# Performance work log

Hardware: AMD Instinct MI355X
Metric: run time of the kernel (lower is better)

Reference implementation:

```python
import jax, jax.numpy as jnp
import numpy as np

N_NODES = 50000
N_EDGES = 600000
D_IN = 256    # hidden_lstm
D_GNN = 128   # hidden_gnn
D_OUT = 1     # out_channels


def setup_inputs() -> dict:
    key = jax.random.key(0)
    ks = jax.random.split(key, 8)
    x = jax.random.normal(ks[0], (N_NODES, D_IN), dtype=jnp.float32)
    edge_index = jax.random.randint(ks[1], (2, N_EDGES), 0, N_NODES, dtype=jnp.int32)
    # SAGEConv params: lin_l applied to aggregated neighbors (with bias), lin_r to root
    s_in = 1.0 / np.sqrt(D_IN)
    W_l = jax.random.uniform(ks[2], (D_IN, D_GNN), jnp.float32, -s_in, s_in)
    b_l = jax.random.uniform(ks[3], (D_GNN,), jnp.float32, -s_in, s_in)
    W_r = jax.random.uniform(ks[4], (D_IN, D_GNN), jnp.float32, -s_in, s_in)
    # fc head
    s_g = 1.0 / np.sqrt(D_GNN)
    W_fc = jax.random.uniform(ks[5], (D_GNN, D_OUT), jnp.float32, -s_g, s_g)
    b_fc = jax.random.uniform(ks[6], (D_OUT,), jnp.float32, -s_g, s_g)
    return {"x": x, "edge_index": edge_index, "W_l": W_l, "b_l": b_l,
            "W_r": W_r, "W_fc": W_fc, "b_fc": b_fc}


def reference(x, edge_index, W_l, b_l, W_r, W_fc, b_fc):
    # SAGEConv, aggr='mean': out = lin_l(mean_{j in N(i)} x_j) + lin_r(x_i)
    src = edge_index[0]  # message source
    dst = edge_index[1]  # message target
    n = x.shape[0]
    agg = jax.ops.segment_sum(x[src], dst, num_segments=n)            # [N, D_IN]
    cnt = jax.ops.segment_sum(jnp.ones((src.shape[0], 1), x.dtype), dst,
                              num_segments=n)                         # [N, 1]
    mean = agg / jnp.maximum(cnt, 1.0)
    h = mean @ W_l + b_l + x @ W_r                                    # [N, D_GNN]
    pred = jax.nn.sigmoid(h @ W_fc + b_fc).squeeze()                  # [N]
    return h, pred
```

## Files before the change

### kernel.cpp

```cpp
#include <hip/hip_runtime.h>
#include <hip/hip_bf16.h>
#include <math.h>

#define N_NODES 50000
#define N_EDGES 600000
#define D_IN 256
#define D_GNN 128
#define CAP 32
#define MAX_OVER 8192
#define LDS_STRIDE 264

typedef short s16x8 __attribute__((ext_vector_type(8)));
typedef float f32x4 __attribute__((ext_vector_type(4)));

__device__ __forceinline__ unsigned short f2bf(float f) {
  unsigned int u = __float_as_uint(f);
  u += 0x7FFFu + ((u >> 16) & 1u);
  return (unsigned short)(u >> 16);
}

__device__ __forceinline__ ushort4 cvt4(float4 a) {
  union { ushort4 u4; __hip_bfloat162 h[2]; } u;
  u.h[0] = __float22bfloat162_rn(make_float2(a.x, a.y));
  u.h[1] = __float22bfloat162_rn(make_float2(a.z, a.w));
  return u.u4;
}

__global__ __launch_bounds__(256) void pack0(
    const float* __restrict__ Wl, const float* __restrict__ Wr,
    ushort* __restrict__ Wcp, int* __restrict__ cursor,
    int* __restrict__ ovcnt) {
  int i = blockIdx.x * 256 + threadIdx.x;
  if (i < N_NODES) cursor[i] = 0;
  if (i == 0) ovcnt[0] = 0;
  if (i < 8192) {
    int q = i & 3, col = (i >> 2) & 255, ks = i >> 10;
    const float* W = (col < 128) ? Wl : Wr;
    int c = col & 127;
    int k0 = ks * 32 + q * 8;
    s16x8 v;
#pragma unroll
    for (int j = 0; j < 8; j++) v[j] = (short)f2bf(W[(k0 + j) * D_GNN + c]);
    *((s16x8*)(Wcp + (size_t)i * 8)) = v;
  }
}

__global__ __launch_bounds__(256) void fill_pad(
    const int* __restrict__ ei, int* __restrict__ cursor,
    int* __restrict__ colp, int* __restrict__ ovcnt, int2* __restrict__ over) {
  int e = blockIdx.x * 256 + threadIdx.x;
  if (e >= N_EDGES) return;
  int src = ei[e];
  int dst = ei[N_EDGES + e];
  int pos = atomicAdd(&cursor[dst], 1);
  if (pos < CAP) {
    colp[dst * CAP + pos] = src;
  } else {
    int o = atomicAdd(ovcnt, 1);
    if (o < MAX_OVER) over[o] = make_int2(dst, src);
  }
}

__global__ __launch_bounds__(512) void mfma_gemm(
    const float* __restrict__ x, const ushort* __restrict__ Wcp,
    const float* __restrict__ b_l, ushort* __restrict__ yb,
    ushort* __restrict__ yrb) {
  __shared__ ushort xs[64 * LDS_STRIDE];
  const int t = threadIdx.x;
  const int n0 = blockIdx.x * 64;

#pragma unroll
  for (int j = 0; j < 8; j++) {
    int idx = t + j * 512;
    int row = idx >> 6, col4 = idx & 63;
    int gn = n0 + row;
    if (gn >= N_NODES) gn = N_NODES - 1;
    float4 v = ((const float4*)x)[(size_t)gn * 64 + col4];
    *((ushort4*)(xs + row * LDS_STRIDE + col4 * 4)) = cvt4(v);
  }
  __syncthreads();

  const int l = t & 63;
  const int w = t >> 6;
  const int wrow = w & 1;
  const int wcol = w >> 1;
  const int lq = l >> 4, l16 = l & 15;

  f32x4 acc[2][4];
#pragma unroll
  for (int a = 0; a < 2; a++)
#pragma unroll
    for (int b = 0; b < 4; b++) acc[a][b] = (f32x4){0.f, 0.f, 0.f, 0.f};

  const ushort* abase[2];
#pragma unroll
  for (int nt = 0; nt < 2; nt++)
    abase[nt] = xs + (wrow * 32 + nt * 16 + l16) * LDS_STRIDE + lq * 8;
  const ushort* bptr[4];
#pragma unroll
  for (int ct = 0; ct < 4; ct++) {
    int col = wcol * 64 + ct * 16 + l16;
    bptr[ct] = Wcp + ((size_t)col * 4 + lq) * 8;
  }

  s16x8 B[4], Bn[4];
#pragma unroll
  for (int ct = 0; ct < 4; ct++) B[ct] = *((const s16x8*)(bptr[ct]));

#pragma unroll
  for (int ks = 0; ks < 8; ks++) {
    s16x8 A[2];
#pragma unroll
    for (int nt = 0; nt < 2; nt++)
      A[nt] = *((const s16x8*)(abase[nt] + ks * 32));
    if (ks < 7) {
#pragma unroll
      for (int ct = 0; ct < 4; ct++)
        Bn[ct] = *((const s16x8*)(bptr[ct] + (size_t)(ks + 1) * 256 * 32));
    }
#pragma unroll
    for (int nt = 0; nt < 2; nt++)
#pragma unroll
      for (int ct = 0; ct < 4; ct++)
        acc[nt][ct] = __builtin_amdgcn_mfma_f32_16x16x32_bf16(
            A[nt], B[ct], acc[nt][ct], 0, 0, 0);
#pragma unroll
    for (int ct = 0; ct < 4; ct++) B[ct] = Bn[ct];
  }

#pragma unroll
  for (int nt = 0; nt < 2; nt++) {
#pragma unroll
    for (int ct = 0; ct < 4; ct++) {
      int gcol = wcol * 64 + ct * 16 + l16;
#pragma unroll
      for (int r = 0; r < 4; r++) {
        int node = n0 + wrow * 32 + nt * 16 + lq * 4 + r;
        if (node < N_NODES) {
          if (gcol < 128)
            yb[(size_t)node * D_GNN + gcol] = f2bf(acc[nt][ct][r]);
          else
            yrb[(size_t)node * D_GNN + (gcol - 128)] =
                f2bf(acc[nt][ct][r] + b_l[gcol - 128]);
        }
      }
    }
  }
}

__global__ __launch_bounds__(256) void gather_pred(
    const int* __restrict__ cursor, const int* __restrict__ colp,
    const int* __restrict__ ovcnt, const int2* __restrict__ over,
    const ushort* __restrict__ yb, const ushort* __restrict__ yrb,
    const float* __restrict__ Wfc, const float* __restrict__ bfc,
    float* __restrict__ h, float* __restrict__ pred) {
  const int node = (blockIdx.x * 256 + threadIdx.x) >> 6;
  const int lane = threadIdx.x & 63;
  if (node >= N_NODES) return;
  const int degt = cursor[node];
  const int m = min(degt, CAP);
  float ax = 0.f, ay = 0.f;
  const unsigned int* y32 = (const unsigned int*)yb;

  int c = (lane < m) ? colp[node * CAP + lane] : 0;
  int j = 0;
  for (; j + 4 <= m; j += 4) {
    int s0 = __shfl(c, j), s1 = __shfl(c, j + 1);
    int s2 = __shfl(c, j + 2), s3 = __shfl(c, j + 3);
    unsigned int v0 = y32[(size_t)s0 * 64 + lane];
    unsigned int v1 = y32[(size_t)s1 * 64 + lane];
    unsigned int v2 = y32[(size_t)s2 * 64 + lane];
    unsigned int v3 = y32[(size_t)s3 * 64 + lane];
    ax += __uint_as_float(v0 << 16) + __uint_as_float(v1 << 16) +
          __uint_as_float(v2 << 16) + __uint_as_float(v3 << 16);
    ay += __uint_as_float(v0 & 0xFFFF0000u) + __uint_as_float(v1 & 0xFFFF0000u) +
          __uint_as_float(v2 & 0xFFFF0000u) + __uint_as_float(v3 & 0xFFFF0000u);
  }
  for (; j < m; j++) {
    int s0 = __shfl(c, j);
    unsigned int v0 = y32[(size_t)s0 * 64 + lane];
    ax += __uint_as_float(v0 << 16);
    ay += __uint_as_float(v0 & 0xFFFF0000u);
  }
  if (degt > CAP) {
    int nov = min(ovcnt[0], MAX_OVER);
    for (int k = 0; k < nov; k++) {
      int2 ov = over[k];
      if (ov.x == node) {
        unsigned int v0 = y32[(size_t)ov.y * 64 + lane];
        ax += __uint_as_float(v0 << 16);
        ay += __uint_as_float(v0 & 0xFFFF0000u);
      }
    }
  }

  const float ic = degt > 0 ? 1.f / (float)degt : 0.f;
  unsigned int yrv = ((const unsigned int*)yrb)[(size_t)node * 64 + lane];
  float h0 = ax * ic + __uint_as_float(yrv << 16);
  float h1 = ay * ic + __uint_as_float(yrv & 0xFFFF0000u);
  float2 hv; hv.x = h0; hv.y = h1;
  ((float2*)h)[(size_t)node * 64 + lane] = hv;
  float s = h0 * Wfc[2 * lane] + h1 * Wfc[2 * lane + 1];
#pragma unroll
  for (int off = 32; off > 0; off >>= 1) s += __shfl_down(s, off);
  if (lane == 0) pred[node] = 1.f / (1.f + expf(-(s + bfc[0])));
}

extern "C" void kernel_launch(void* const* d_in, const int* in_sizes, int n_in,
                              void* d_out, int out_size, void* d_ws,
                              size_t ws_size, hipStream_t stream) {
  const float* x   = (const float*)d_in[0];
  const int*   ei  = (const int*)d_in[1];
  const float* Wl  = (const float*)d_in[2];
  const float* bl  = (const float*)d_in[3];
  const float* Wr  = (const float*)d_in[4];
  const float* Wfc = (const float*)d_in[5];
  const float* bfc = (const float*)d_in[6];

  float* out  = (float*)d_out;
  float* h    = out;
  float* pred = out + (size_t)N_NODES * D_GNN;

  ushort* Wcp   = (ushort*)d_ws;
  ushort* yb    = Wcp + 8192 * 8;
  ushort* yrb   = yb + (size_t)N_NODES * D_GNN;
  int*   cursor = (int*)(yrb + (size_t)N_NODES * D_GNN);
  int*   ovcnt  = cursor + N_NODES;
  int2*  over   = (int2*)(ovcnt + 1);
  int*   colp   = (int*)(over + MAX_OVER);

  pack0<<<(N_NODES + 255) / 256, 256, 0, stream>>>(Wl, Wr, Wcp, cursor, ovcnt);

  fill_pad<<<(N_EDGES + 255) / 256, 256, 0, stream>>>(ei, cursor, colp, ovcnt,
                                                      over);

  mfma_gemm<<<(N_NODES + 63) / 64, 512, 0, stream>>>(x, Wcp, bl, yb, yrb);

  gather_pred<<<(N_NODES * 64 + 255) / 256, 256, 0, stream>>>(
      cursor, colp, ovcnt, over, yb, yrb, Wfc, bfc, h, pred);
}
```

Before: 185.7 us.

## Stage fp32 x tile into LDS via direct global-to-LDS loads with XOR swizzle

```diff
diff --git a/kernel.cpp b/kernel.cpp
--- a/kernel.cpp
+++ b/kernel.cpp
@@ -8,7 +8,6 @@
 #define D_GNN 128
 #define CAP 32
 #define MAX_OVER 8192
-#define LDS_STRIDE 264
 
 typedef short s16x8 __attribute__((ext_vector_type(8)));
 typedef float f32x4 __attribute__((ext_vector_type(4)));
@@ -61,27 +60,29 @@
   }
 }
 
-__global__ __launch_bounds__(512) void mfma_gemm(
+__global__ __launch_bounds__(512, 4) void mfma_gemm(
     const float* __restrict__ x, const ushort* __restrict__ Wcp,
     const float* __restrict__ b_l, ushort* __restrict__ yb,
     ushort* __restrict__ yrb) {
-  __shared__ ushort xs[64 * LDS_STRIDE];
+  __shared__ float xs[64 * 256];
   const int t = threadIdx.x;
   const int n0 = blockIdx.x * 64;
+  const int l = t & 63;
+  const int w = t >> 6;
 
 #pragma unroll
   for (int j = 0; j < 8; j++) {
-    int idx = t + j * 512;
-    int row = idx >> 6, col4 = idx & 63;
+    const int row = j * 8 + w;
     int gn = n0 + row;
     if (gn >= N_NODES) gn = N_NODES - 1;
-    float4 v = ((const float4*)x)[(size_t)gn * 64 + col4];
-    *((ushort4*)(xs + row * LDS_STRIDE + col4 * 4)) = cvt4(v);
-  }
-  __syncthreads();
-
-  const int l = t & 63;
-  const int w = t >> 6;
+    const int sc = (l & ~7) | ((l & 7) ^ (row & 7));
+    __builtin_amdgcn_global_load_lds(
+        (const __attribute__((address_space(1))) unsigned int*)(
+            x + (size_t)gn * 256 + sc * 4),
+        (__attribute__((address_space(3))) unsigned int*)(xs + row * 256),
+        16, 0, 0);
+  }
+
   const int wrow = w & 1;
   const int wcol = w >> 1;
   const int lq = l >> 4, l16 = l & 15;
@@ -92,10 +93,15 @@
 #pragma unroll
     for (int b = 0; b < 4; b++) acc[a][b] = (f32x4){0.f, 0.f, 0.f, 0.f};
 
-  const ushort* abase[2];
-#pragma unroll
-  for (int nt = 0; nt < 2; nt++)
-    abase[nt] = xs + (wrow * 32 + nt * 16 + l16) * LDS_STRIDE + lq * 8;
+  const float* ap0[2];
+  const float* ap1[2];
+#pragma unroll
+  for (int nt = 0; nt < 2; nt++) {
+    int rl = wrow * 32 + nt * 16 + l16;
+    int o0 = (lq * 2) ^ (rl & 7);
+    ap0[nt] = xs + rl * 256 + o0 * 4;
+    ap1[nt] = xs + rl * 256 + (o0 ^ 1) * 4;
+  }
   const ushort* bptr[4];
 #pragma unroll
   for (int ct = 0; ct < 4; ct++) {
@@ -107,12 +113,20 @@
 #pragma unroll
   for (int ct = 0; ct < 4; ct++) B[ct] = *((const s16x8*)(bptr[ct]));
 
+  __syncthreads();
+
 #pragma unroll
   for (int ks = 0; ks < 8; ks++) {
     s16x8 A[2];
 #pragma unroll
-    for (int nt = 0; nt < 2; nt++)
-      A[nt] = *((const s16x8*)(abase[nt] + ks * 32));
+    for (int nt = 0; nt < 2; nt++) {
+      float4 a0 = *((const float4*)(ap0[nt] + ks * 32));
+      float4 a1 = *((const float4*)(ap1[nt] + ks * 32));
+      union { s16x8 v; ushort4 u[2]; } ua;
+      ua.u[0] = cvt4(a0);
+      ua.u[1] = cvt4(a1);
+      A[nt] = ua.v;
+    }
     if (ks < 7) {
 #pragma unroll
       for (int ct = 0; ct < 4; ct++)
```

Result: slower. 193.4 us (+4.2%).
